# Kernel tuning notes

Hardware: AMD Instinct MI355X
Metric: run time of the kernel (lower is better)

## Reference

```python
import jax, jax.numpy as jnp
import numpy as np

N = 50000
E = 800000
IN_DIM, HID_DIM, OUT_DIM = 128, 64, 32


def _gcn_layer(x, src, dst, norm, W, b, n):
    # GCNConv: h = D^{-1/2}(A+I)D^{-1/2} (x W) + b
    h = x @ W  # [n, d_out]
    agg = jax.ops.segment_sum(h[src] * norm[:, None], dst, num_segments=n)
    return agg + b


def _backbone(x, edge_index, W1, b1, W2, b2):
    n = x.shape[0]
    loop = jnp.arange(n)
    src = jnp.concatenate([edge_index[0], loop])  # add self-loops
    dst = jnp.concatenate([edge_index[1], loop])
    deg = jax.ops.segment_sum(jnp.ones(src.shape[0], x.dtype), dst, num_segments=n)
    dinv = jax.lax.rsqrt(deg)  # deg >= 1 thanks to self-loops
    norm = dinv[src] * dinv[dst]  # symmetric normalization per edge
    h = jax.nn.relu(_gcn_layer(x, src, dst, norm, W1, b1, n))
    return _gcn_layer(h, src, dst, norm, W2, b2, n)


def _zscore_cols(h):
    # torch: (h - h.mean(0)) / h.std(0), std is unbiased (ddof=1)
    mean = h.mean(0)
    std = jnp.sqrt(jnp.sum((h - mean) ** 2, axis=0) / (h.shape[0] - 1))
    return (h - mean) / std


def setup_inputs() -> dict:
    key = jax.random.key(0)
    k1, k2, k3, k4, k5, k6 = jax.random.split(key, 6)
    x1 = jax.random.normal(k1, (N, IN_DIM), dtype=jnp.float32)
    x2 = jax.random.normal(k2, (N, IN_DIM), dtype=jnp.float32)
    edge_index1 = jax.random.randint(k3, (2, E), 0, N, dtype=jnp.int64 if jax.config.jax_enable_x64 else jnp.int32)
    edge_index2 = jax.random.randint(k4, (2, E), 0, N, dtype=jnp.int64 if jax.config.jax_enable_x64 else jnp.int32)
    W1 = jax.random.normal(k5, (IN_DIM, HID_DIM), dtype=jnp.float32) * (1.0 / np.sqrt(IN_DIM))
    W2 = jax.random.normal(k6, (HID_DIM, OUT_DIM), dtype=jnp.float32) * (1.0 / np.sqrt(HID_DIM))
    b1 = jnp.zeros((HID_DIM,), jnp.float32)
    b2 = jnp.zeros((OUT_DIM,), jnp.float32)
    return {"x1": x1, "edge_index1": edge_index1, "x2": x2, "edge_index2": edge_index2,
            "W1": W1, "b1": b1, "W2": W2, "b2": b2}


def reference(x1, edge_index1, x2, edge_index2, W1, b1, W2, b2):
    h1 = _backbone(x1, edge_index1, W1, b1, W2, b2)
    h2 = _backbone(x2, edge_index2, W1, b1, W2, b2)
    z1 = _zscore_cols(h1)
    z2 = _zscore_cols(h2)
    return (z1, z2)
```

## Files before the change

kernel.cpp:

```cpp
#include <hip/hip_runtime.h>
#include <hip/hip_fp16.h>
#include <math.h>

#define IN_DIM 128
#define HID 64
#define OUTD 32
#define BSH 8
#define BSZ 256
#define EPB 4096
#define XPAD 136
#define NCOPY 16

typedef __attribute__((ext_vector_type(8))) _Float16 f16x8;
typedef __attribute__((ext_vector_type(4))) float f32x4;

struct GB {
    const int* src; const int* dst;
    int* bh;
    int* btot;
    int* boff;
    unsigned int* pairs;
    int* rowptr; int* csr_src;
    float* dinv;
    double* st;
    float* og;
    const float* x;
    _Float16* hs;
    __half* h2;
};

__global__ void __launch_bounds__(256) k_p1(GB g0, GB g1, const float* __restrict__ W,
                                            int e, int n, int nb, int nbh, int nmm) {
    __shared__ char smem[2 * 64 * XPAD * 2];
    int tid = threadIdx.x;
    int bx = blockIdx.x;
    if (bx < 2 * nbh) {
        const GB& g = (bx >= nbh) ? g1 : g0;
        int blk = (bx >= nbh) ? bx - nbh : bx;
        int* hist = (int*)smem;
        for (int i = tid; i < nb; i += 256) hist[i] = 0;
        __syncthreads();
        int base = blk * EPB;
#pragma unroll
        for (int k = 0; k < EPB / 256; ++k) {
            int idx = base + k * 256 + tid;
            if (idx < e) atomicAdd(&hist[g.dst[idx] >> BSH], 1);
        }
        __syncthreads();
        int* row = g.bh + (size_t)blk * nb;
        for (int i = tid; i < nb; i += 256) row[i] = hist[i];
    } else {
        int mx = bx - 2 * nbh;
        const GB& g = (mx >= nmm) ? g1 : g0;
        int blk = (mx >= nmm) ? mx - nmm : mx;
        _Float16 (*xs)[XPAD] = (_Float16(*)[XPAD])smem;
        _Float16 (*wt)[XPAD] = (_Float16(*)[XPAD])(smem + 64 * XPAD * 2);
        int node0 = blk * 64;
        {
            const float4* W4 = (const float4*)W;
#pragma unroll
            for (int j = 0; j < 8; ++j) {
                int idx4 = tid + 256 * j;
                float4 w = W4[idx4];
                int k = idx4 >> 4;
                int d = (idx4 & 15) * 4;
                wt[d][k]     = (_Float16)w.x;
                wt[d + 1][k] = (_Float16)w.y;
                wt[d + 2][k] = (_Float16)w.z;
                wt[d + 3][k] = (_Float16)w.w;
            }
        }
        {
            const float4* X4 = (const float4*)g.x;
#pragma unroll
            for (int j = 0; j < 8; ++j) {
                int i = tid + 256 * j;
                int row = i >> 5, c4 = i & 31;
                int gn = node0 + row;
                float4 v = (gn < n) ? X4[(size_t)gn * 32 + c4] : make_float4(0.f, 0.f, 0.f, 0.f);
                _Float16* p = &xs[row][c4 * 4];
                p[0] = (_Float16)v.x; p[1] = (_Float16)v.y;
                p[2] = (_Float16)v.z; p[3] = (_Float16)v.w;
            }
        }
        __syncthreads();
        int wv = tid >> 6, lane = tid & 63;
        int r16 = lane & 15, khi = lane >> 4;
        int wnode0 = wv * 16;
        f32x4 acc[4] = {};
#pragma unroll
        for (int kk = 0; kk < 4; ++kk) {
            f16x8 a = *(const f16x8*)&xs[wnode0 + r16][kk * 32 + khi * 8];
#pragma unroll
            for (int nt = 0; nt < 4; ++nt) {
                f16x8 b = *(const f16x8*)&wt[nt * 16 + r16][kk * 32 + khi * 8];
                acc[nt] = __builtin_amdgcn_mfma_f32_16x16x32_f16(a, b, acc[nt], 0, 0, 0);
            }
        }
#pragma unroll
        for (int r = 0; r < 4; ++r) {
            int node = node0 + wnode0 + khi * 4 + r;
            if (node < n) {
#pragma unroll
                for (int nt = 0; nt < 4; ++nt)
                    g.hs[(size_t)node * HID + nt * 16 + r16] = (_Float16)acc[nt][r];
            }
        }
    }
}

__global__ void k_colscan(GB g0, GB g1, int nb, int nbh) {
    const GB& g = blockIdx.y ? g1 : g0;
    __shared__ int ls[256];
    int tid = threadIdx.x;
    int b = blockIdx.x;
    int v = (tid < nbh) ? g.bh[(size_t)tid * nb + b] : 0;
    ls[tid] = v;
    __syncthreads();
    for (int off = 1; off < 256; off <<= 1) {
        int u = (tid >= off) ? ls[tid - off] : 0;
        __syncthreads();
        ls[tid] += u;
        __syncthreads();
    }
    if (tid < nbh) g.bh[(size_t)tid * nb + b] = ls[tid] - v;
    if (tid == 255) g.btot[b] = ls[255];
}

__global__ void k_scan_btot(GB g0, GB g1, int nb) {
    const GB& g = blockIdx.y ? g1 : g0;
    __shared__ int ls[1024];
    int tid = threadIdx.x;
    int v = (tid < nb) ? g.btot[tid] : 0;
    ls[tid] = v;
    __syncthreads();
    for (int off = 1; off < 1024; off <<= 1) {
        int u = (tid >= off) ? ls[tid - off] : 0;
        __syncthreads();
        ls[tid] += u;
        __syncthreads();
    }
    if (tid < nb) g.boff[tid] = ls[tid] - v;
    g.st[tid] = 0.0;
}

__global__ void k_part2(GB g0, GB g1, int e, int nb) {
    const GB& g = blockIdx.y ? g1 : g0;
    __shared__ int lcur[512];
    int tid = threadIdx.x;
    const int* row = g.bh + (size_t)blockIdx.x * nb;
    for (int i = tid; i < nb; i += 256) lcur[i] = g.boff[i] + row[i];
    __syncthreads();
    int base = blockIdx.x * EPB;
#pragma unroll
    for (int k = 0; k < EPB / 256; ++k) {
        int idx = base + k * 256 + tid;
        if (idx < e) {
            int s = g.src[idx], d = g.dst[idx];
            int pos = atomicAdd(&lcur[d >> BSH], 1);
            g.pairs[pos] = (unsigned int)s | ((unsigned int)(d & (BSZ - 1)) << 24);
        }
    }
}

__global__ void k_local_csr(GB g0, GB g1, int n, int e) {
    const GB& g = blockIdx.y ? g1 : g0;
    __shared__ int ldeg[BSZ], lrow[BSZ];
    __shared__ float ldv[BSZ];
    int tid = threadIdx.x;
    int b = blockIdx.x;
    int node0 = b << BSH;
    int lo = g.boff[b], hi = lo + g.btot[b];
    ldeg[tid] = 0;
    __syncthreads();
    for (int j = lo + tid; j < hi; j += 256)
        atomicAdd(&ldeg[g.pairs[j] >> 24], 1);
    __syncthreads();
    int d = ldeg[tid];
    lrow[tid] = d;
    __syncthreads();
    for (int off = 1; off < BSZ; off <<= 1) {
        int u = (tid >= off) ? lrow[tid - off] : 0;
        __syncthreads();
        lrow[tid] += u;
        __syncthreads();
    }
    int node = node0 + tid;
    if (node < n) {
        g.rowptr[node] = lo + lrow[tid] - d;
        float dvv = rsqrtf((float)(d + 1));
        g.dinv[node] = dvv;
        ldv[tid] = dvv;
    } else {
        ldv[tid] = 0.0f;
    }
    lrow[tid] = lo + lrow[tid] - d;
    __syncthreads();
    for (int j = lo + tid; j < hi; j += 256) {
        unsigned int w = g.pairs[j];
        int pos = atomicAdd(&lrow[w >> 24], 1);
        g.csr_src[pos] = (int)(w & 0xFFFFFFu);
    }
    if (b == 0 && tid == 0) g.rowptr[n] = e;
    __half2* Hv = (__half2*)g.hs;
    for (int i = tid; i < BSZ * (HID / 2); i += 256) {
        int row = i >> 5;
        int nd = node0 + row;
        if (nd < n) {
            float sc = ldv[row];
            size_t idx = (size_t)nd * (HID / 2) + (i & 31);
            float2 v = __half22float2(Hv[idx]);
            Hv[idx] = __floats2half2_rn(v.x * sc, v.y * sc);
        }
    }
}

__global__ void __launch_bounds__(256) k_gather_fuse(GB g0, GB g1, const float* __restrict__ b1,
                                                     const float* __restrict__ W2, int n, int nblkg) {
    int bx = blockIdx.x;
    const GB& g = ((bx & 7) >= 4) ? g1 : g0;
    int blk = (bx >> 3) * 4 + (bx & 3);
    if (blk >= nblkg) return;
    __shared__ float sh[32][HID + 1];
    __shared__ float w2s[HID][OUTD];
    __shared__ float bs[HID];
    int tid = threadIdx.x;
    for (int i = tid; i < HID * OUTD; i += 256) w2s[i >> 5][i & 31] = W2[i];
    if (tid < HID) bs[tid] = b1[tid];
    int l8 = tid & 7, gi = tid >> 3;
    int node = blk * 32 + gi;
    float a[8] = {};
    if (node < n) {
        const f16x8* H = (const f16x8*)g.hs;
        f16x8 v = H[(size_t)node * 8 + l8];
#pragma unroll
        for (int k = 0; k < 8; ++k) a[k] = (float)v[k];
        int lo = g.rowptr[node], hi = g.rowptr[node + 1];
        int j = lo;
        for (; j + 8 <= hi; j += 8) {
            int s0 = g.csr_src[j],     s1 = g.csr_src[j + 1];
            int s2 = g.csr_src[j + 2], s3 = g.csr_src[j + 3];
            int s4 = g.csr_src[j + 4], s5 = g.csr_src[j + 5];
            int s6 = g.csr_src[j + 6], s7 = g.csr_src[j + 7];
            f16x8 v0 = H[(size_t)s0 * 8 + l8];
            f16x8 v1 = H[(size_t)s1 * 8 + l8];
            f16x8 v2 = H[(size_t)s2 * 8 + l8];
            f16x8 v3 = H[(size_t)s3 * 8 + l8];
            f16x8 v4 = H[(size_t)s4 * 8 + l8];
            f16x8 v5 = H[(size_t)s5 * 8 + l8];
            f16x8 v6 = H[(size_t)s6 * 8 + l8];
            f16x8 v7 = H[(size_t)s7 * 8 + l8];
            f16x8 s01 = v0 + v1, s23 = v2 + v3, s45 = v4 + v5, s67 = v6 + v7;
            f16x8 s = (s01 + s23) + (s45 + s67);
#pragma unroll
            for (int k = 0; k < 8; ++k) a[k] += (float)s[k];
        }
        if (j + 4 <= hi) {
            int s0 = g.csr_src[j],     s1 = g.csr_src[j + 1];
            int s2 = g.csr_src[j + 2], s3 = g.csr_src[j + 3];
            f16x8 v0 = H[(size_t)s0 * 8 + l8];
            f16x8 v1 = H[(size_t)s1 * 8 + l8];
            f16x8 v2 = H[(size_t)s2 * 8 + l8];
            f16x8 v3 = H[(size_t)s3 * 8 + l8];
            f16x8 s = (v0 + v1) + (v2 + v3);
#pragma unroll
            for (int k = 0; k < 8; ++k) a[k] += (float)s[k];
            j += 4;
        }
        for (; j < hi; ++j) {
            f16x8 v0 = H[(size_t)g.csr_src[j] * 8 + l8];
#pragma unroll
            for (int k = 0; k < 8; ++k) a[k] += (float)v0[k];
        }
    }
    __syncthreads();
    if (node < n) {
        float dv = g.dinv[node];
#pragma unroll
        for (int k = 0; k < 8; ++k)
            a[k] = fmaxf(fmaf(a[k], dv, bs[l8 * 8 + k]), 0.0f);
    }
#pragma unroll
    for (int k = 0; k < 8; ++k) sh[gi][l8 * 8 + k] = a[k];
    __syncthreads();
    int n2 = tid >> 3, fo = (tid & 7) * 4;
    int node2 = blk * 32 + n2;
    if (node2 < n) {
        float a0 = 0.f, a1 = 0.f, a2 = 0.f, a3 = 0.f;
#pragma unroll
        for (int k = 0; k < HID; ++k) {
            float s = sh[n2][k];
            a0 = fmaf(s, w2s[k][fo], a0);
            a1 = fmaf(s, w2s[k][fo + 1], a1);
            a2 = fmaf(s, w2s[k][fo + 2], a2);
            a3 = fmaf(s, w2s[k][fo + 3], a3);
        }
        float dv2 = g.dinv[node2];
        __half2* H2 = (__half2*)g.h2;
        H2[(size_t)node2 * (OUTD / 2) + (fo >> 1)]     = __floats2half2_rn(a0 * dv2, a1 * dv2);
        H2[(size_t)node2 * (OUTD / 2) + (fo >> 1) + 1] = __floats2half2_rn(a2 * dv2, a3 * dv2);
    }
}

__global__ void __launch_bounds__(256) k_gather2s(GB g0, GB g1, int n, int nblkg) {
    int bx = blockIdx.x;
    const GB& g = ((bx & 7) >= 4) ? g1 : g0;
    int blk = (bx >> 3) * 4 + (bx & 3);
    if (blk >= nblkg) return;
    __shared__ float sx[64][33], sq[64][33];
    int tid = threadIdx.x;
    int l4 = tid & 3, gi = tid >> 2;
    int node = blk * 64 + gi;
    float a[8] = {};
    if (node < n) {
        const f16x8* H = (const f16x8*)g.h2;
        f16x8 v = H[(size_t)node * 4 + l4];
#pragma unroll
        for (int k = 0; k < 8; ++k) a[k] = (float)v[k];
        int lo = g.rowptr[node], hi = g.rowptr[node + 1];
        int j = lo;
        for (; j + 8 <= hi; j += 8) {
            int s0 = g.csr_src[j],     s1 = g.csr_src[j + 1];
            int s2 = g.csr_src[j + 2], s3 = g.csr_src[j + 3];
            int s4 = g.csr_src[j + 4], s5 = g.csr_src[j + 5];
            int s6 = g.csr_src[j + 6], s7 = g.csr_src[j + 7];
            f16x8 v0 = H[(size_t)s0 * 4 + l4];
            f16x8 v1 = H[(size_t)s1 * 4 + l4];
            f16x8 v2 = H[(size_t)s2 * 4 + l4];
            f16x8 v3 = H[(size_t)s3 * 4 + l4];
            f16x8 v4 = H[(size_t)s4 * 4 + l4];
            f16x8 v5 = H[(size_t)s5 * 4 + l4];
            f16x8 v6 = H[(size_t)s6 * 4 + l4];
            f16x8 v7 = H[(size_t)s7 * 4 + l4];
            f16x8 s01 = v0 + v1, s23 = v2 + v3, s45 = v4 + v5, s67 = v6 + v7;
            f16x8 s = (s01 + s23) + (s45 + s67);
#pragma unroll
            for (int k = 0; k < 8; ++k) a[k] += (float)s[k];
        }
        if (j + 4 <= hi) {
            int s0 = g.csr_src[j],     s1 = g.csr_src[j + 1];
            int s2 = g.csr_src[j + 2], s3 = g.csr_src[j + 3];
            f16x8 v0 = H[(size_t)s0 * 4 + l4];
            f16x8 v1 = H[(size_t)s1 * 4 + l4];
            f16x8 v2 = H[(size_t)s2 * 4 + l4];
            f16x8 v3 = H[(size_t)s3 * 4 + l4];
            f16x8 s = (v0 + v1) + (v2 + v3);
#pragma unroll
            for (int k = 0; k < 8; ++k) a[k] += (float)s[k];
            j += 4;
        }
        for (; j < hi; ++j) {
            f16x8 v0 = H[(size_t)g.csr_src[j] * 4 + l4];
#pragma unroll
            for (int k = 0; k < 8; ++k) a[k] += (float)v0[k];
        }
        float dv = g.dinv[node];
#pragma unroll
        for (int k = 0; k < 8; ++k) a[k] *= dv;
        float4* O4 = (float4*)g.og;
        O4[(size_t)node * 8 + l4 * 2]     = make_float4(a[0], a[1], a[2], a[3]);
        O4[(size_t)node * 8 + l4 * 2 + 1] = make_float4(a[4], a[5], a[6], a[7]);
    }
#pragma unroll
    for (int k = 0; k < 8; ++k) {
        sx[gi][l4 * 8 + k] = a[k];
        sq[gi][l4 * 8 + k] = a[k] * a[k];
    }
    __syncthreads();
    if (tid < 64) {
        int c = tid & 31;
        bool isq = tid >= 32;
        float s = 0.0f;
        for (int r = 0; r < 64; ++r) s += isq ? sq[r][c] : sx[r][c];
        atomicAdd(&g.st[(blk & (NCOPY - 1)) * 64 + c + (isq ? 32 : 0)], (double)s);
    }
}

__global__ void k_transform(GB g0, GB g1, int n) {
    const GB& g = blockIdx.y ? g1 : g0;
    __shared__ float fm[32], fr[32];
    int tid = threadIdx.x;
    if (tid < 32) {
        double sum = 0.0, sqs = 0.0;
#pragma unroll
        for (int k = 0; k < NCOPY; ++k) {
            sum += g.st[k * 64 + tid];
            sqs += g.st[k * 64 + tid + 32];
        }
        double mean = sum / (double)n;
        double var = (sqs - sum * sum / (double)n) / (double)(n - 1);
        fm[tid] = (float)mean;
        fr[tid] = (float)(1.0 / sqrt(var));
    }
    __syncthreads();
    int t = blockIdx.x * 256 + tid;
    if (t < n * OUTD) {
        int c = t & 31;
        g.og[t] = (g.og[t] - fm[c]) * fr[c];
    }
}


extern "C" void kernel_launch(void* const* d_in, const int* in_sizes, int n_in,
                              void* d_out, int out_size, void* d_ws, size_t ws_size,
                              hipStream_t stream) {
    const float* x1 = (const float*)d_in[0];
    const int*   ei1 = (const int*)d_in[1];
    const float* x2 = (const float*)d_in[2];
    const int*   ei2 = (const int*)d_in[3];
    const float* W1 = (const float*)d_in[4];
    const float* b1 = (const float*)d_in[5];
    const float* W2 = (const float*)d_in[6];
    const float* b2 = (const float*)d_in[7];
    (void)b2;
    (void)n_in; (void)out_size; (void)ws_size;

    int n = in_sizes[0] / IN_DIM;
    int e = in_sizes[1] / 2;
    float* out = (float*)d_out;
    int nb  = (n + BSZ - 1) >> BSH;
    int nbh = (e + EPB - 1) / EPB;
    int nmm = (n + 63) / 64;

    char* ws = (char*)d_ws;
    size_t off = 0;
    auto alloc = [&](size_t bytes) {
        void* p = ws + off;
        off = (off + bytes + 255) & ~(size_t)255;
        return p;
    };
    int*    bh_base   = (int*)alloc((size_t)2 * nbh * nb * 4);
    int*    btot_base = (int*)alloc((size_t)2 * nb * 4);
    int*    boff_base = (int*)alloc((size_t)2 * nb * 4);
    double* st_base   = (double*)alloc((size_t)2 * NCOPY * 64 * 8);

    GB G[2];
    for (int g = 0; g < 2; ++g) {
        const int* ei = g ? ei2 : ei1;
        G[g].src  = ei;
        G[g].dst  = ei + e;
        G[g].x    = g ? x2 : x1;
        G[g].bh   = bh_base + (size_t)g * nbh * nb;
        G[g].btot = btot_base + (size_t)g * nb;
        G[g].boff = boff_base + (size_t)g * nb;
        G[g].st   = st_base + (size_t)g * NCOPY * 64;
        G[g].rowptr  = (int*)alloc(((size_t)n + 1) * 4);
        G[g].csr_src = (int*)alloc((size_t)e * 4);
        G[g].dinv    = (float*)alloc((size_t)n * 4);
        G[g].og      = out + (size_t)g * n * OUTD;
        G[g].hs      = (_Float16*)alloc((size_t)n * HID * 2);
    }
    size_t pairs_bytes = (size_t)2 * e * 4;
    size_t h2_bytes    = (size_t)2 * n * OUTD * 2;
    char* uni = (char*)alloc(pairs_bytes > h2_bytes ? pairs_bytes : h2_bytes);
    G[0].pairs = (unsigned int*)uni;
    G[1].pairs = G[0].pairs + e;
    G[0].h2 = (__half*)uni;
    G[1].h2 = G[0].h2 + (size_t)n * OUTD;

    k_p1<<<dim3(2 * nbh + 2 * nmm), 256, 0, stream>>>(G[0], G[1], W1, e, n, nb, nbh, nmm);
    k_colscan<<<dim3(nb, 2), 256, 0, stream>>>(G[0], G[1], nb, nbh);
    k_scan_btot<<<dim3(1, 2), 1024, 0, stream>>>(G[0], G[1], nb);
    k_part2<<<dim3(nbh, 2), 256, 0, stream>>>(G[0], G[1], e, nb);
    k_local_csr<<<dim3(nb, 2), BSZ, 0, stream>>>(G[0], G[1], n, e);

    int nblkg1 = (n + 31) / 32;
    int slots1 = ((nblkg1 + 3) / 4) * 8;
    k_gather_fuse<<<dim3(slots1), 256, 0, stream>>>(G[0], G[1], b1, W2, n, nblkg1);
    int nblkg2 = (n + 63) / 64;
    int slots2 = ((nblkg2 + 3) / 4) * 8;
    k_gather2s<<<dim3(slots2), 256, 0, stream>>>(G[0], G[1], n, nblkg2);

    k_transform<<<dim3((n * OUTD + 255) / 256, 2), 256, 0, stream>>>(G[0], G[1], n);
}
```

Measured before the change: 132.8 us.

## Fold bucket-offset scan into partition kernels and stage final output in fp16

Removes the separate single-block scan kernel: each k_part2 and k_local_csr block now recomputes the exclusive scan of bucket totals in shared memory, and zeroing of the stats buffer moves into k_colscan. Both kernels use interleaved graph-slot indexing instead of a 2D grid. The second-layer gather writes an fp16 intermediate rather than fp32 into the output, and the z-score transform reads that fp16 and writes four floats per thread. This drops one launch and cuts intermediate memory traffic, at the cost of redundant scans per block and reduced precision of the pre-normalization values. The in-block scan assumes nb ≤ 256.

```diff
diff --git a/kernel.cpp b/kernel.cpp
--- a/kernel.cpp
+++ b/kernel.cpp
@@ -18,12 +18,12 @@
     const int* src; const int* dst;
     int* bh;
     int* btot;
-    int* boff;
     unsigned int* pairs;
     int* rowptr; int* csr_src;
     float* dinv;
     double* st;
     float* og;
+    _Float16* o16;
     const float* x;
     _Float16* hs;
     __half* h2;
@@ -125,33 +125,37 @@
     }
     if (tid < nbh) g.bh[(size_t)tid * nb + b] = ls[tid] - v;
     if (tid == 255) g.btot[b] = ls[255];
-}
-
-__global__ void k_scan_btot(GB g0, GB g1, int nb) {
-    const GB& g = blockIdx.y ? g1 : g0;
-    __shared__ int ls[1024];
+    if (b < 4) {
+        int i = b * 256 + tid;
+        g.st[i] = 0.0;
+    }
+}
+
+__global__ void __launch_bounds__(256) k_part2(GB g0, GB g1, int e, int nb, int nbh) {
+    int bx = blockIdx.x;
+    const GB& g = ((bx & 7) >= 4) ? g1 : g0;
+    int blk = (bx >> 3) * 4 + (bx & 3);
+    if (blk >= nbh) return;
+    __shared__ int sc[256];
+    __shared__ int lcur[512];
     int tid = threadIdx.x;
     int v = (tid < nb) ? g.btot[tid] : 0;
-    ls[tid] = v;
-    __syncthreads();
-    for (int off = 1; off < 1024; off <<= 1) {
-        int u = (tid >= off) ? ls[tid - off] : 0;
-        __syncthreads();
-        ls[tid] += u;
-        __syncthreads();
-    }
-    if (tid < nb) g.boff[tid] = ls[tid] - v;
-    g.st[tid] = 0.0;
-}
-
-__global__ void k_part2(GB g0, GB g1, int e, int nb) {
-    const GB& g = blockIdx.y ? g1 : g0;
-    __shared__ int lcur[512];
-    int tid = threadIdx.x;
-    const int* row = g.bh + (size_t)blockIdx.x * nb;
-    for (int i = tid; i < nb; i += 256) lcur[i] = g.boff[i] + row[i];
-    __syncthreads();
-    int base = blockIdx.x * EPB;
+    sc[tid] = v;
+    __syncthreads();
+    for (int off = 1; off < 256; off <<= 1) {
+        int u = (tid >= off) ? sc[tid - off] : 0;
+        __syncthreads();
+        sc[tid] += u;
+        __syncthreads();
+    }
+    int excl = sc[tid] - v;
+    __syncthreads();
+    sc[tid] = excl;
+    __syncthreads();
+    const int* row = g.bh + (size_t)blk * nb;
+    for (int i = tid; i < nb; i += 256) lcur[i] = sc[i] + row[i];
+    __syncthreads();
+    int base = blk * EPB;
 #pragma unroll
     for (int k = 0; k < EPB / 256; ++k) {
         int idx = base + k * 256 + tid;
@@ -163,14 +167,29 @@
     }
 }
 
-__global__ void k_local_csr(GB g0, GB g1, int n, int e) {
-    const GB& g = blockIdx.y ? g1 : g0;
-    __shared__ int ldeg[BSZ], lrow[BSZ];
+__global__ void __launch_bounds__(256) k_local_csr(GB g0, GB g1, int n, int e, int nb) {
+    int bx = blockIdx.x;
+    const GB& g = ((bx & 7) >= 4) ? g1 : g0;
+    int b = (bx >> 3) * 4 + (bx & 3);
+    if (b >= nb) return;
+    __shared__ int sc[256], ldeg[BSZ], lrow[BSZ];
     __shared__ float ldv[BSZ];
     int tid = threadIdx.x;
-    int b = blockIdx.x;
+    int v = (tid < nb) ? g.btot[tid] : 0;
+    sc[tid] = v;
+    __syncthreads();
+    for (int off = 1; off < 256; off <<= 1) {
+        int u = (tid >= off) ? sc[tid - off] : 0;
+        __syncthreads();
+        sc[tid] += u;
+        __syncthreads();
+    }
+    int excl = sc[tid] - v;
+    __syncthreads();
+    sc[tid] = excl;
+    __syncthreads();
     int node0 = b << BSH;
-    int lo = g.boff[b], hi = lo + g.btot[b];
+    int lo = sc[b], hi = lo + g.btot[b];
     ldeg[tid] = 0;
     __syncthreads();
     for (int j = lo + tid; j < hi; j += 256)
@@ -207,10 +226,10 @@
         int row = i >> 5;
         int nd = node0 + row;
         if (nd < n) {
-            float sc = ldv[row];
+            float scv = ldv[row];
             size_t idx = (size_t)nd * (HID / 2) + (i & 31);
-            float2 v = __half22float2(Hv[idx]);
-            Hv[idx] = __floats2half2_rn(v.x * sc, v.y * sc);
+            float2 vv = __half22float2(Hv[idx]);
+            Hv[idx] = __floats2half2_rn(vv.x * scv, vv.y * scv);
         }
     }
 }
@@ -357,9 +376,10 @@
         float dv = g.dinv[node];
 #pragma unroll
         for (int k = 0; k < 8; ++k) a[k] *= dv;
-        float4* O4 = (float4*)g.og;
-        O4[(size_t)node * 8 + l4 * 2]     = make_float4(a[0], a[1], a[2], a[3]);
-        O4[(size_t)node * 8 + l4 * 2 + 1] = make_float4(a[4], a[5], a[6], a[7]);
+        f16x8 o;
+#pragma unroll
+        for (int k = 0; k < 8; ++k) o[k] = (_Float16)a[k];
+        ((f16x8*)g.o16)[(size_t)node * 4 + l4] = o;
     }
 #pragma unroll
     for (int k = 0; k < 8; ++k) {
@@ -393,10 +413,18 @@
         fr[tid] = (float)(1.0 / sqrt(var));
     }
     __syncthreads();
-    int t = blockIdx.x * 256 + tid;
-    if (t < n * OUTD) {
-        int c = t & 31;
-        g.og[t] = (g.og[t] - fm[c]) * fr[c];
+    int t4 = (blockIdx.x * 256 + tid) * 4;
+    if (t4 < n * OUTD) {
+        const __half2* O = (const __half2*)g.o16;
+        float2 u0 = __half22float2(O[t4 / 2]);
+        float2 u1 = __half22float2(O[t4 / 2 + 1]);
+        int c = t4 & 31;
+        float4 r;
+        r.x = (u0.x - fm[c])     * fr[c];
+        r.y = (u0.y - fm[c + 1]) * fr[c + 1];
+        r.z = (u1.x - fm[c + 2]) * fr[c + 2];
+        r.w = (u1.y - fm[c + 3]) * fr[c + 3];
+        *(float4*)&g.og[t4] = r;
     }
 }
 
@@ -431,8 +459,8 @@
     };
     int*    bh_base   = (int*)alloc((size_t)2 * nbh * nb * 4);
     int*    btot_base = (int*)alloc((size_t)2 * nb * 4);
-    int*    boff_base = (int*)alloc((size_t)2 * nb * 4);
     double* st_base   = (double*)alloc((size_t)2 * NCOPY * 64 * 8);
+    _Float16* o16_base = (_Float16*)alloc((size_t)2 * n * OUTD * 2);
 
     GB G[2];
     for (int g = 0; g < 2; ++g) {
@@ -442,8 +470,8 @@
         G[g].x    = g ? x2 : x1;
         G[g].bh   = bh_base + (size_t)g * nbh * nb;
         G[g].btot = btot_base + (size_t)g * nb;
-        G[g].boff = boff_base + (size_t)g * nb;
         G[g].st   = st_base + (size_t)g * NCOPY * 64;
+        G[g].o16  = o16_base + (size_t)g * n * OUTD;
         G[g].rowptr  = (int*)alloc(((size_t)n + 1) * 4);
         G[g].csr_src = (int*)alloc((size_t)e * 4);
         G[g].dinv    = (float*)alloc((size_t)n * 4);
@@ -460,9 +488,10 @@
 
     k_p1<<<dim3(2 * nbh + 2 * nmm), 256, 0, stream>>>(G[0], G[1], W1, e, n, nb, nbh, nmm);
     k_colscan<<<dim3(nb, 2), 256, 0, stream>>>(G[0], G[1], nb, nbh);
-    k_scan_btot<<<dim3(1, 2), 1024, 0, stream>>>(G[0], G[1], nb);
-    k_part2<<<dim3(nbh, 2), 256, 0, stream>>>(G[0], G[1], e, nb);
-    k_local_csr<<<dim3(nb, 2), BSZ, 0, stream>>>(G[0], G[1], n, e);
+    int slotsP = ((nbh + 3) / 4) * 8;
+    k_part2<<<dim3(slotsP), 256, 0, stream>>>(G[0], G[1], e, nb, nbh);
+    int slotsC = ((nb + 3) / 4) * 8;
+    k_local_csr<<<dim3(slotsC), BSZ, 0, stream>>>(G[0], G[1], n, e, nb);
 
     int nblkg1 = (n + 31) / 32;
     int slots1 = ((nblkg1 + 3) / 4) * 8;
@@ -471,5 +500,5 @@
     int slots2 = ((nblkg2 + 3) / 4) * 8;
     k_gather2s<<<dim3(slots2), 256, 0, stream>>>(G[0], G[1], n, nblkg2);
 
-    k_transform<<<dim3((n * OUTD + 255) / 256, 2), 256, 0, stream>>>(G[0], G[1], n);
-}
+    k_transform<<<dim3((n * OUTD / 4 + 255) / 256, 2), 256, 0, stream>>>(G[0], G[1], n);
+}
```

Measured after the change: 121.5 us. 1.09x faster.
